# Performance work log

Hardware: AMD Instinct MI355X
Metric: run time of the kernel (lower is better)

Reference implementation:

```python
import jax, jax.numpy as jnp
import numpy as np

N = 50000
E = 800000
H = 128
L = 3
EPS_BN = 1e-5
EPS_NORM = 1e-12
NEG_SLOPE = 0.1


def setup_inputs() -> dict:
    key = jax.random.key(0)
    ks = jax.random.split(key, 10)
    s = 1.0 / np.sqrt(H)
    x = jax.random.normal(ks[0], (N, H), dtype=jnp.float32)
    edge_index = jax.random.randint(ks[1], (2, E), 0, N, dtype=jnp.int64)
    # per-layer SAGEConv params: lin_l (neighbors, with bias), lin_r (root, no bias)
    Wl = jax.random.uniform(ks[2], (L, H, H), jnp.float32, -s, s)
    bl = jax.random.uniform(ks[3], (L, H), jnp.float32, -s, s)
    Wr = jax.random.uniform(ks[4], (L, H, H), jnp.float32, -s, s)
    # BatchNorm affine params per layer
    gamma = jnp.ones((L, H), jnp.float32)
    beta = jnp.zeros((L, H), jnp.float32)
    # shared skip linear
    Ws = jax.random.uniform(ks[5], (H, H), jnp.float32, -s, s)
    bs = jax.random.uniform(ks[6], (H,), jnp.float32, -s, s)
    return {"x": x, "edge_index": edge_index, "Wl": Wl, "bl": bl, "Wr": Wr,
            "gamma": gamma, "beta": beta, "Ws": Ws, "bs": bs}


def _layer(x, src, dst, Wl, bl, Wr, g, b, Ws, bs):
    # skip residual
    res = x @ Ws.T + bs
    # SAGEConv mean aggregation: messages src -> dst
    agg = jax.ops.segment_sum(x[src], dst, num_segments=N)  # [N,H]
    deg = jax.ops.segment_sum(jnp.ones((E,), x.dtype), dst, num_segments=N)
    agg = agg / jnp.maximum(deg, 1.0)[:, None]
    out = agg @ Wl.T + bl + x @ Wr.T
    # normalize=True -> L2 normalize over features
    nrm = jnp.sqrt(jnp.sum(out * out, axis=-1, keepdims=True))
    out = out / jnp.maximum(nrm, EPS_NORM)
    # BatchNorm over nodes (batch statistics)
    mu = out.mean(axis=0)
    var = out.var(axis=0)
    out = (out - mu) * jax.lax.rsqrt(var + EPS_BN) * g + b
    # LeakyReLU(0.1); dropout is identity in eval
    out = jnp.where(out >= 0, out, NEG_SLOPE * out)
    return out + res


def reference(x, edge_index, Wl, bl, Wr, gamma, beta, Ws, bs):
    src, dst = edge_index[0], edge_index[1]
    for l in range(L):
        x = _layer(x, src, dst, Wl[l], bl[l], Wr[l], gamma[l], beta[l], Ws, bs)
    return x
```

## Files before the change

kernel.cpp:

```cpp
#include <hip/hip_runtime.h>
#include <hip/hip_bf16.h>
#include <stdint.h>

#define NN 50000
#define NE 800000
#define HD 128
#define NL 3
#define EPS_BN 1e-5f
#define EPS_NORM 1e-12f
#define NEG_SLOPE 0.1f

#define SCAN_CHUNK 256
#define SCAN_BLOCKS ((NN + SCAN_CHUNK - 1) / SCAN_CHUNK)
#define NTILES ((NN + 127) / 128)

#define BSH 9
#define NB ((NN + (1 << BSH) - 1) >> BSH)
#define MAXBE 9728

typedef __attribute__((ext_vector_type(8))) short bf16x8;
typedef __attribute__((ext_vector_type(4))) float f32x4;

static __device__ __forceinline__ unsigned pack_bf16(float a, float b) {
  unsigned ua = __builtin_bit_cast(unsigned, a);
  unsigned ub = __builtin_bit_cast(unsigned, b);
  ua = (ua + 0x7fffu + ((ua >> 16) & 1u)) >> 16;
  ub = (ub + 0x7fffu + ((ub >> 16) & 1u)) >> 16;
  return ua | (ub << 16);
}
static __device__ __forceinline__ ushort bf16of(float f) {
  unsigned u = __builtin_bit_cast(unsigned, f);
  u = (u + 0x7fffu + ((u >> 16) & 1u)) >> 16;
  return (ushort)u;
}
static __device__ __forceinline__ float bflo(unsigned u) { return __builtin_bit_cast(float, u << 16); }
static __device__ __forceinline__ float bfhi(unsigned u) { return __builtin_bit_cast(float, u & 0xffff0000u); }

__global__ __launch_bounds__(256) void hist_kernel(const int* __restrict__ dst, int* __restrict__ degi) {
  int i = blockIdx.x * 256 + threadIdx.x;
  if (i < NE) atomicAdd(&degi[dst[i]], 1);
}

__global__ __launch_bounds__(256) void blocksum_kernel(const int* __restrict__ degi,
                                                       int* __restrict__ blocksum) {
  __shared__ int sh[256];
  int t = threadIdx.x;
  int i = blockIdx.x * 256 + t;
  sh[t] = (i < NN) ? degi[i] : 0;
  __syncthreads();
  for (int off = 128; off >= 1; off >>= 1) {
    if (t < off) sh[t] += sh[t + off];
    __syncthreads();
  }
  if (t == 0) blocksum[blockIdx.x] = sh[0];
}

__global__ __launch_bounds__(256) void blockscan_kernel(int* __restrict__ blocksum,
                                                        int* __restrict__ blockoff,
                                                        int* __restrict__ rowptr) {
  __shared__ int sh[256];
  int t = threadIdx.x;
  int v = (t < SCAN_BLOCKS) ? blocksum[t] : 0;
  sh[t] = v;
  __syncthreads();
  for (int off = 1; off < 256; off <<= 1) {
    int u = (t >= off) ? sh[t - off] : 0;
    __syncthreads();
    sh[t] += u;
    __syncthreads();
  }
  if (t < SCAN_BLOCKS) blockoff[t] = sh[t] - v;
  if (t == 255) rowptr[NN] = sh[255];
}

__global__ __launch_bounds__(256) void chunkscan_kernel(const int* __restrict__ degi,
                                                        const int* __restrict__ blockoff,
                                                        int* __restrict__ rowptr,
                                                        int* __restrict__ bcursor,
                                                        float* __restrict__ invdeg) {
  __shared__ int sh[256];
  int t = threadIdx.x;
  int i = blockIdx.x * 256 + t;
  int d = (i < NN) ? degi[i] : 0;
  sh[t] = d;
  __syncthreads();
  for (int off = 1; off < 256; off <<= 1) {
    int u = (t >= off) ? sh[t - off] : 0;
    __syncthreads();
    sh[t] += u;
    __syncthreads();
  }
  if (i < NN) {
    int pre = blockoff[blockIdx.x] + sh[t] - d;
    rowptr[i] = pre;
    if ((i & ((1 << BSH) - 1)) == 0) bcursor[i >> BSH] = pre;
    invdeg[i] = 1.0f / fmaxf((float)d, 1.0f);
  }
}

__global__ __launch_bounds__(1024) void bucketB_kernel(const int* __restrict__ src,
                                                       const int* __restrict__ dst,
                                                       int* __restrict__ bcursor,
                                                       uint2* __restrict__ bpack) {
  __shared__ int hist[NB], lstart[NB], gbase[NB];
  __shared__ uint2 sdat[1024];
  const int tid = threadIdx.x;
  const int e = blockIdx.x * 1024 + tid;
  if (tid < NB) hist[tid] = 0;
  __syncthreads();
  int s = 0, d = 0, b = 0, myIdx = 0;
  bool valid = (e < NE);
  if (valid) {
    s = src[e];
    d = dst[e];
    b = d >> BSH;
    myIdx = atomicAdd(&hist[b], 1);
  }
  __syncthreads();
  if (tid == 0) {
    int run = 0;
    for (int i = 0; i < NB; ++i) { lstart[i] = run; run += hist[i]; }
  }
  __syncthreads();
  if (tid < NB && hist[tid] > 0) gbase[tid] = atomicAdd(&bcursor[tid], hist[tid]);
  __syncthreads();
  if (valid) sdat[lstart[b] + myIdx] = make_uint2((unsigned)s, (unsigned)d);
  __syncthreads();
  int tot = lstart[NB - 1] + hist[NB - 1];
  if (tid < tot) {
    uint2 p = sdat[tid];
    int bb = (int)(p.y >> BSH);
    bpack[gbase[bb] + (tid - lstart[bb])] = p;
  }
}

__global__ __launch_bounds__(1024) void bucketC_kernel(const int* __restrict__ rowptr,
                                                       const uint2* __restrict__ bpack,
                                                       int* __restrict__ esrc) {
  __shared__ int lcur[1 << BSH];
  __shared__ int lsrc[MAXBE];
  const int c = blockIdx.x, tid = threadIdx.x;
  const int nbase = c << BSH;
  const int nend = min(nbase + (1 << BSH), NN);
  const int ebase = rowptr[nbase];
  const int cnt = rowptr[nend] - ebase;
  if (tid < (1 << BSH)) {
    int n = nbase + tid;
    lcur[tid] = (n < nend) ? rowptr[n] - ebase : 0;
  }
  __syncthreads();
  for (int i = tid; i < cnt; i += 1024) {
    uint2 p = bpack[ebase + i];
    int pos = atomicAdd(&lcur[(int)p.y - nbase], 1);
    if (pos < MAXBE) lsrc[pos] = (int)p.x;
  }
  __syncthreads();
  for (int i = tid; i < cnt; i += 1024) esrc[ebase + i] = lsrc[i];
}

__global__ __launch_bounds__(256) void tobf16_kernel(const float* __restrict__ x, ushort* __restrict__ xb) {
  int i = blockIdx.x * 256 + threadIdx.x;
  if (i < NN * 64) {
    float2 f = *(const float2*)(x + (size_t)i * 2);
    *(unsigned*)(xb + (size_t)i * 2) = pack_bf16(f.x, f.y);
  }
}

__global__ __launch_bounds__(256) void packW_kernel(const float* __restrict__ Wl,
                                                    const float* __restrict__ Wr,
                                                    const float* __restrict__ Wsm,
                                                    unsigned* __restrict__ wpackL,
                                                    unsigned* __restrict__ wpackS) {
  int i = blockIdx.x * 256 + threadIdx.x;
  if (i < NL * 16384) {
    int l = i >> 14, rem = i & 16383;
    int c = rem >> 7, kp = rem & 127;
    int k2 = kp * 2;
    float f0, f1;
    if (k2 < HD) { const float* W = Wl + (size_t)l * HD * HD + c * HD + k2; f0 = W[0]; f1 = W[1]; }
    else         { const float* W = Wr + (size_t)l * HD * HD + c * HD + (k2 - HD); f0 = W[0]; f1 = W[1]; }
    unsigned ba = (unsigned)(c * 512 + kp * 4) ^ (unsigned)((c & 7) << 4);
    *(unsigned*)((char*)(wpackL + (size_t)l * 16384) + ba) = pack_bf16(f0, f1);
  } else if (i < NL * 16384 + 8192) {
    int j = i - NL * 16384;
    int c = j >> 6, kp = j & 63;
    int k2 = kp * 2;
    unsigned ba = (unsigned)(c * 256 + kp * 4) ^ (unsigned)((c & 7) << 4);
    *(unsigned*)((char*)wpackS + ba) = pack_bf16(Wsm[c * HD + k2], Wsm[c * HD + k2 + 1]);
  }
}

__global__ __launch_bounds__(512) void agg_csr_kernel(const ushort* __restrict__ xb,
                                                      const int* __restrict__ rowptr,
                                                      const int* __restrict__ esrc,
                                                      const float* __restrict__ invdeg,
                                                      ushort* __restrict__ aggb,
                                                      float* __restrict__ colsum,
                                                      float* __restrict__ colsumsq) {
  if (blockIdx.x == 0 && threadIdx.x < 2 * HD) {
    if (threadIdx.x < HD) colsum[threadIdx.x] = 0.f;
    else colsumsq[threadIdx.x - HD] = 0.f;
  }
  int wid = (blockIdx.x * 512 + threadIdx.x) >> 6;
  int lane = threadIdx.x & 63;
  int node = wid * 4 + (lane >> 4);
  int sub = lane & 15;
  if (node >= NN) return;
  int start = rowptr[node], end = rowptr[node + 1];
  float a0 = 0.f, a1 = 0.f, a2 = 0.f, a3 = 0.f, a4 = 0.f, a5 = 0.f, a6 = 0.f, a7 = 0.f;
  int e = start;
  for (; e + 4 <= end; e += 4) {
    int s0 = esrc[e], s1 = esrc[e + 1], s2 = esrc[e + 2], s3 = esrc[e + 3];
    uint4 u0 = *(const uint4*)((const char*)xb + (size_t)s0 * 256 + sub * 16);
    uint4 u1 = *(const uint4*)((const char*)xb + (size_t)s1 * 256 + sub * 16);
    uint4 u2 = *(const uint4*)((const char*)xb + (size_t)s2 * 256 + sub * 16);
    uint4 u3 = *(const uint4*)((const char*)xb + (size_t)s3 * 256 + sub * 16);
    a0 += (bflo(u0.x) + bflo(u1.x)) + (bflo(u2.x) + bflo(u3.x));
    a1 += (bfhi(u0.x) + bfhi(u1.x)) + (bfhi(u2.x) + bfhi(u3.x));
    a2 += (bflo(u0.y) + bflo(u1.y)) + (bflo(u2.y) + bflo(u3.y));
    a3 += (bfhi(u0.y) + bfhi(u1.y)) + (bfhi(u2.y) + bfhi(u3.y));
    a4 += (bflo(u0.z) + bflo(u1.z)) + (bflo(u2.z) + bflo(u3.z));
    a5 += (bfhi(u0.z) + bfhi(u1.z)) + (bfhi(u2.z) + bfhi(u3.z));
    a6 += (bflo(u0.w) + bflo(u1.w)) + (bflo(u2.w) + bflo(u3.w));
    a7 += (bfhi(u0.w) + bfhi(u1.w)) + (bfhi(u2.w) + bfhi(u3.w));
  }
  for (; e < end; ++e) {
    uint4 u = *(const uint4*)((const char*)xb + (size_t)esrc[e] * 256 + sub * 16);
    a0 += bflo(u.x); a1 += bfhi(u.x);
    a2 += bflo(u.y); a3 += bfhi(u.y);
    a4 += bflo(u.z); a5 += bfhi(u.z);
    a6 += bflo(u.w); a7 += bfhi(u.w);
  }
  float id = invdeg[node];
  uint4 o;
  o.x = pack_bf16(a0 * id, a1 * id);
  o.y = pack_bf16(a2 * id, a3 * id);
  o.z = pack_bf16(a4 * id, a5 * id);
  o.w = pack_bf16(a6 * id, a7 * id);
  *(uint4*)((char*)aggb + (size_t)node * 256 + sub * 16) = o;
}

__global__ __launch_bounds__(512, 4) void mfma_pre_kernel(
    const ushort* __restrict__ aggb, const ushort* __restrict__ xb,
    const unsigned* __restrict__ wpackL, const float* __restrict__ bl,
    uint4* __restrict__ prebn,
    float* __restrict__ colsum, float* __restrict__ colsumsq) {
  __shared__ unsigned Bsw[16384];
  __shared__ float lsum[HD], lsq[HD];
  const int tid = threadIdx.x;
  {
    const uint4* s = (const uint4*)wpackL;
    uint4* d = (uint4*)Bsw;
#pragma unroll
    for (int i = 0; i < 8; ++i) d[tid + i * 512] = s[tid + i * 512];
  }
  if (tid < HD) { lsum[tid] = 0.f; lsq[tid] = 0.f; }

  const int wave = tid >> 6, lane = tid & 63;
  const int lhi = lane >> 4, llo = lane & 15;
  int arow = blockIdx.x * 128 + wave * 16 + llo;
  if (arow >= NN) arow = NN - 1;
  const size_t rb = (size_t)arow * 256;

  uint4 areg[8];
#pragma unroll
  for (int ks = 0; ks < 4; ++ks) {
    areg[ks]     = *(const uint4*)((const char*)aggb + rb + ks * 64 + lhi * 16);
    areg[ks + 4] = *(const uint4*)((const char*)xb   + rb + ks * 64 + lhi * 16);
  }

  f32x4 acc[8];
#pragma unroll
  for (int ct = 0; ct < 8; ++ct) {
    float b = bl[ct * 16 + llo];
    acc[ct] = (f32x4){b, b, b, b};
  }
  __syncthreads();

#pragma unroll
  for (int ks = 0; ks < 8; ++ks) {
    bf16x8 a = __builtin_bit_cast(bf16x8, areg[ks]);
#pragma unroll
    for (int ct = 0; ct < 8; ++ct) {
      int bcol = ct * 16 + llo;
      unsigned bb = (unsigned)(bcol * 512 + ks * 64 + lhi * 16) ^ (unsigned)((bcol & 7) << 4);
      bf16x8 b = *(const bf16x8*)((const char*)Bsw + bb);
      acc[ct] = __builtin_amdgcn_mfma_f32_16x16x32_bf16(a, b, acc[ct], 0, 0, 0);
    }
  }

  float cs[8] = {0, 0, 0, 0, 0, 0, 0, 0}, cq[8] = {0, 0, 0, 0, 0, 0, 0, 0};
#pragma unroll
  for (int r = 0; r < 4; ++r) {
    int orow = blockIdx.x * 128 + wave * 16 + lhi * 4 + r;
    float p[8];
    float ss = 0.f;
#pragma unroll
    for (int ct = 0; ct < 8; ++ct) { p[ct] = acc[ct][r]; ss += p[ct] * p[ct]; }
#pragma unroll
    for (int m = 8; m >= 1; m >>= 1) ss += __shfl_xor(ss, m, 64);
    float inv = 1.0f / fmaxf(sqrtf(ss), EPS_NORM);
#pragma unroll
    for (int ct = 0; ct < 8; ++ct) p[ct] *= inv;
    uint4 o;
    o.x = pack_bf16(p[0], p[1]);
    o.y = pack_bf16(p[2], p[3]);
    o.z = pack_bf16(p[4], p[5]);
    o.w = pack_bf16(p[6], p[7]);
    prebn[((size_t)blockIdx.x * 32 + wave * 4 + r) * 64 + lane] = o;
    if (orow < NN) {
#pragma unroll
      for (int ct = 0; ct < 8; ++ct) { cs[ct] += p[ct]; cq[ct] += p[ct] * p[ct]; }
    }
  }
#pragma unroll
  for (int ct = 0; ct < 8; ++ct) {
    atomicAdd(&lsum[ct * 16 + llo], cs[ct]);
    atomicAdd(&lsq[ct * 16 + llo], cq[ct]);
  }
  __syncthreads();
  if (tid < HD) {
    atomicAdd(&colsum[tid], lsum[tid]);
    atomicAdd(&colsumsq[tid], lsq[tid]);
  }
}

__global__ __launch_bounds__(512, 4) void res_mfma_kernel(
    ushort* __restrict__ xb, const uint4* __restrict__ prebn,
    const unsigned* __restrict__ wpackS, const float* __restrict__ bs,
    const float* __restrict__ colsum, const float* __restrict__ colsumsq,
    const float* __restrict__ gamma, const float* __restrict__ beta,
    float* __restrict__ outf, int last) {
  __shared__ unsigned Bsw[8192];
  __shared__ float lscale[HD], lshift[HD];
  const int tid = threadIdx.x;
  {
    const uint4* s = (const uint4*)wpackS;
    uint4* d = (uint4*)Bsw;
#pragma unroll
    for (int i = 0; i < 4; ++i) d[tid + i * 512] = s[tid + i * 512];
  }
  if (tid < HD) {
    float mu = colsum[tid] * (1.0f / NN);
    float ex2 = colsumsq[tid] * (1.0f / NN);
    float var = ex2 - mu * mu;
    float sc = gamma[tid] * rsqrtf(var + EPS_BN);
    lscale[tid] = sc;
    lshift[tid] = beta[tid] - mu * sc;
  }

  const int wave = tid >> 6, lane = tid & 63;
  const int lhi = lane >> 4, llo = lane & 15;
  int arow = blockIdx.x * 128 + wave * 16 + llo;
  if (arow >= NN) arow = NN - 1;
  const size_t rb = (size_t)arow * 256;

  uint4 areg[4];
#pragma unroll
  for (int ks = 0; ks < 4; ++ks)
    areg[ks] = *(const uint4*)((const char*)xb + rb + ks * 64 + lhi * 16);
  uint4 pv4[4];
#pragma unroll
  for (int r = 0; r < 4; ++r)
    pv4[r] = prebn[((size_t)blockIdx.x * 32 + wave * 4 + r) * 64 + lane];

  f32x4 acc[8];
#pragma unroll
  for (int ct = 0; ct < 8; ++ct) {
    float b = bs[ct * 16 + llo];
    acc[ct] = (f32x4){b, b, b, b};
  }
  __syncthreads();

  float sc8[8], sh8[8];
#pragma unroll
  for (int ct = 0; ct < 8; ++ct) {
    int C = ct * 16 + llo;
    sc8[ct] = lscale[C];
    sh8[ct] = lshift[C];
  }

#pragma unroll
  for (int ks = 0; ks < 4; ++ks) {
    bf16x8 a = __builtin_bit_cast(bf16x8, areg[ks]);
#pragma unroll
    for (int ct = 0; ct < 8; ++ct) {
      int bcol = ct * 16 + llo;
      unsigned bb = (unsigned)(bcol * 256 + ks * 64 + lhi * 16) ^ (unsigned)((bcol & 7) << 4);
      bf16x8 b = *(const bf16x8*)((const char*)Bsw + bb);
      acc[ct] = __builtin_amdgcn_mfma_f32_16x16x32_bf16(a, b, acc[ct], 0, 0, 0);
    }
  }

#pragma unroll
  for (int r = 0; r < 4; ++r) {
    int orow = blockIdx.x * 128 + wave * 16 + lhi * 4 + r;
    if (orow < NN) {
      const unsigned* pw = (const unsigned*)&pv4[r];
#pragma unroll
      for (int ct = 0; ct < 8; ++ct) {
        unsigned w = pw[ct >> 1];
        float pv = (ct & 1) ? bfhi(w) : bflo(w);
        float v = pv * sc8[ct] + sh8[ct];
        v = v >= 0.f ? v : NEG_SLOPE * v;
        float o = v + acc[ct][r];
        if (last) outf[(size_t)orow * HD + ct * 16 + llo] = o;
        else      xb[(size_t)orow * HD + ct * 16 + llo] = bf16of(o);
      }
    }
  }
}

extern "C" void kernel_launch(void* const* d_in, const int* in_sizes, int n_in,
                              void* d_out, int out_size, void* d_ws, size_t ws_size,
                              hipStream_t stream) {
  const float* x0    = (const float*)d_in[0];
  const int*   ei    = (const int*)d_in[1];
  const float* Wl    = (const float*)d_in[2];
  const float* bl    = (const float*)d_in[3];
  const float* Wr    = (const float*)d_in[4];
  const float* gamma = (const float*)d_in[5];
  const float* beta  = (const float*)d_in[6];
  const float* Wsm   = (const float*)d_in[7];
  const float* bs    = (const float*)d_in[8];
  float* out = (float*)d_out;

  char* w = (char*)d_ws;
  ushort* aggb = (ushort*)w;        w += (size_t)NN * HD * 2;
  ushort* xb   = (ushort*)w;        w += (size_t)NN * HD * 2;
  uint4* prebn = (uint4*)w;         w += (size_t)NTILES * 32 * 64 * 16;
  unsigned* wpackL = (unsigned*)w;  w += (size_t)NL * 16384 * 4;
  unsigned* wpackS = (unsigned*)w;  w += 8192 * 4;
  float* invdeg = (float*)w;        w += (size_t)NN * 4;
  float* colsum = (float*)w;        w += HD * 4;
  float* colsumsq = (float*)w;      w += HD * 4;
  int* degi = (int*)w;              w += (size_t)NN * 4;
  int* rowptr = (int*)w;            w += (size_t)(NN + 1) * 4;
  int* bcursor = (int*)w;           w += (size_t)(NB + 8) * 4;
  int* blocksum = (int*)w;          w += SCAN_BLOCKS * 4;
  int* blockoff = (int*)w;          w += SCAN_BLOCKS * 4;
  uint2* bpack = (uint2*)w;         w += (size_t)NE * 8;
  int* esrc = (int*)w;              w += (size_t)NE * 4;

  const int* srcp = ei;
  const int* dstp = ei + NE;

  hipMemsetAsync(degi, 0, NN * sizeof(int), stream);
  hist_kernel<<<(NE + 255) / 256, 256, 0, stream>>>(dstp, degi);
  blocksum_kernel<<<SCAN_BLOCKS, 256, 0, stream>>>(degi, blocksum);
  blockscan_kernel<<<1, 256, 0, stream>>>(blocksum, blockoff, rowptr);
  chunkscan_kernel<<<SCAN_BLOCKS, 256, 0, stream>>>(degi, blockoff, rowptr, bcursor, invdeg);
  bucketB_kernel<<<(NE + 1023) / 1024, 1024, 0, stream>>>(srcp, dstp, bcursor, bpack);
  bucketC_kernel<<<NB, 1024, 0, stream>>>(rowptr, bpack, esrc);
  tobf16_kernel<<<(NN * 64 + 255) / 256, 256, 0, stream>>>(x0, xb);
  packW_kernel<<<(NL * 16384 + 8192 + 255) / 256, 256, 0, stream>>>(Wl, Wr, Wsm, wpackL, wpackS);

  const int aggBlocks = (((NN + 3) / 4) * 64 + 511) / 512;
  for (int l = 0; l < NL; ++l) {
    agg_csr_kernel<<<aggBlocks, 512, 0, stream>>>(xb, rowptr, esrc, invdeg, aggb,
                                                  colsum, colsumsq);
    mfma_pre_kernel<<<NTILES, 512, 0, stream>>>(aggb, xb, wpackL + (size_t)l * 16384,
                                                bl + (size_t)l * HD, prebn, colsum, colsumsq);
    res_mfma_kernel<<<NTILES, 512, 0, stream>>>(xb, prebn, wpackS, bs,
                                                colsum, colsumsq,
                                                gamma + (size_t)l * HD, beta + (size_t)l * HD,
                                                out, l == NL - 1 ? 1 : 0);
  }
}
```

Baseline: 306.9 us.

## Fuse CSR neighbor aggregation into the MFMA pre-BN kernel via shared memory

The separate aggregation kernel is removed. Each 128-row tile block now gathers its neighbor means directly into the first half of its shared buffer, with an XOR swizzle, and then loads its A operands from there. This drops the global write and re-read of the bf16 aggregate buffer and one launch per layer. The second half of the weights is staged first, and the first half is loaded after the aggregate tile has been consumed, which adds an extra barrier. Column-sum zeroing moves to one upfront memset of per-layer stats buffers. Fewer gather waves run concurrently, since the block count is now limited to one block per tile, which could hurt latency hiding for the irregular gathers.

```diff
diff --git a/kernel.cpp b/kernel.cpp
--- a/kernel.cpp
+++ b/kernel.cpp
@@ -190,83 +190,92 @@
   }
 }
 
-__global__ __launch_bounds__(512) void agg_csr_kernel(const ushort* __restrict__ xb,
-                                                      const int* __restrict__ rowptr,
-                                                      const int* __restrict__ esrc,
-                                                      const float* __restrict__ invdeg,
-                                                      ushort* __restrict__ aggb,
-                                                      float* __restrict__ colsum,
-                                                      float* __restrict__ colsumsq) {
-  if (blockIdx.x == 0 && threadIdx.x < 2 * HD) {
-    if (threadIdx.x < HD) colsum[threadIdx.x] = 0.f;
-    else colsumsq[threadIdx.x - HD] = 0.f;
-  }
-  int wid = (blockIdx.x * 512 + threadIdx.x) >> 6;
-  int lane = threadIdx.x & 63;
-  int node = wid * 4 + (lane >> 4);
-  int sub = lane & 15;
-  if (node >= NN) return;
-  int start = rowptr[node], end = rowptr[node + 1];
-  float a0 = 0.f, a1 = 0.f, a2 = 0.f, a3 = 0.f, a4 = 0.f, a5 = 0.f, a6 = 0.f, a7 = 0.f;
-  int e = start;
-  for (; e + 4 <= end; e += 4) {
-    int s0 = esrc[e], s1 = esrc[e + 1], s2 = esrc[e + 2], s3 = esrc[e + 3];
-    uint4 u0 = *(const uint4*)((const char*)xb + (size_t)s0 * 256 + sub * 16);
-    uint4 u1 = *(const uint4*)((const char*)xb + (size_t)s1 * 256 + sub * 16);
-    uint4 u2 = *(const uint4*)((const char*)xb + (size_t)s2 * 256 + sub * 16);
-    uint4 u3 = *(const uint4*)((const char*)xb + (size_t)s3 * 256 + sub * 16);
-    a0 += (bflo(u0.x) + bflo(u1.x)) + (bflo(u2.x) + bflo(u3.x));
-    a1 += (bfhi(u0.x) + bfhi(u1.x)) + (bfhi(u2.x) + bfhi(u3.x));
-    a2 += (bflo(u0.y) + bflo(u1.y)) + (bflo(u2.y) + bflo(u3.y));
-    a3 += (bfhi(u0.y) + bfhi(u1.y)) + (bfhi(u2.y) + bfhi(u3.y));
-    a4 += (bflo(u0.z) + bflo(u1.z)) + (bflo(u2.z) + bflo(u3.z));
-    a5 += (bfhi(u0.z) + bfhi(u1.z)) + (bfhi(u2.z) + bfhi(u3.z));
-    a6 += (bflo(u0.w) + bflo(u1.w)) + (bflo(u2.w) + bflo(u3.w));
-    a7 += (bfhi(u0.w) + bfhi(u1.w)) + (bfhi(u2.w) + bfhi(u3.w));
-  }
-  for (; e < end; ++e) {
-    uint4 u = *(const uint4*)((const char*)xb + (size_t)esrc[e] * 256 + sub * 16);
-    a0 += bflo(u.x); a1 += bfhi(u.x);
-    a2 += bflo(u.y); a3 += bfhi(u.y);
-    a4 += bflo(u.z); a5 += bfhi(u.z);
-    a6 += bflo(u.w); a7 += bfhi(u.w);
-  }
-  float id = invdeg[node];
-  uint4 o;
-  o.x = pack_bf16(a0 * id, a1 * id);
-  o.y = pack_bf16(a2 * id, a3 * id);
-  o.z = pack_bf16(a4 * id, a5 * id);
-  o.w = pack_bf16(a6 * id, a7 * id);
-  *(uint4*)((char*)aggb + (size_t)node * 256 + sub * 16) = o;
-}
-
-__global__ __launch_bounds__(512, 4) void mfma_pre_kernel(
-    const ushort* __restrict__ aggb, const ushort* __restrict__ xb,
+__global__ __launch_bounds__(512, 4) void fused_pre_kernel(
+    const ushort* __restrict__ xb, const int* __restrict__ rowptr,
+    const int* __restrict__ esrc, const float* __restrict__ invdeg,
     const unsigned* __restrict__ wpackL, const float* __restrict__ bl,
     uint4* __restrict__ prebn,
     float* __restrict__ colsum, float* __restrict__ colsumsq) {
   __shared__ unsigned Bsw[16384];
   __shared__ float lsum[HD], lsq[HD];
   const int tid = threadIdx.x;
+  const int r0 = blockIdx.x * 128;
+
   {
     const uint4* s = (const uint4*)wpackL;
     uint4* d = (uint4*)Bsw;
 #pragma unroll
-    for (int i = 0; i < 8; ++i) d[tid + i * 512] = s[tid + i * 512];
+    for (int i = 0; i < 4; ++i) d[2048 + tid + i * 512] = s[2048 + tid + i * 512];
   }
   if (tid < HD) { lsum[tid] = 0.f; lsq[tid] = 0.f; }
 
   const int wave = tid >> 6, lane = tid & 63;
+
+  {
+    const int sub = lane & 15;
+#pragma unroll
+    for (int pass = 0; pass < 4; ++pass) {
+      int nl = pass * 32 + wave * 4 + (lane >> 4);
+      int node = r0 + nl;
+      uint4 o = make_uint4(0u, 0u, 0u, 0u);
+      if (node < NN) {
+        int start = rowptr[node], end = rowptr[node + 1];
+        float a0 = 0.f, a1 = 0.f, a2 = 0.f, a3 = 0.f, a4 = 0.f, a5 = 0.f, a6 = 0.f, a7 = 0.f;
+        int e = start;
+        for (; e + 4 <= end; e += 4) {
+          int s0 = esrc[e], s1 = esrc[e + 1], s2 = esrc[e + 2], s3 = esrc[e + 3];
+          uint4 u0 = *(const uint4*)((const char*)xb + (size_t)s0 * 256 + sub * 16);
+          uint4 u1 = *(const uint4*)((const char*)xb + (size_t)s1 * 256 + sub * 16);
+          uint4 u2 = *(const uint4*)((const char*)xb + (size_t)s2 * 256 + sub * 16);
+          uint4 u3 = *(const uint4*)((const char*)xb + (size_t)s3 * 256 + sub * 16);
+          a0 += (bflo(u0.x) + bflo(u1.x)) + (bflo(u2.x) + bflo(u3.x));
+          a1 += (bfhi(u0.x) + bfhi(u1.x)) + (bfhi(u2.x) + bfhi(u3.x));
+          a2 += (bflo(u0.y) + bflo(u1.y)) + (bflo(u2.y) + bflo(u3.y));
+          a3 += (bfhi(u0.y) + bfhi(u1.y)) + (bfhi(u2.y) + bfhi(u3.y));
+          a4 += (bflo(u0.z) + bflo(u1.z)) + (bflo(u2.z) + bflo(u3.z));
+          a5 += (bfhi(u0.z) + bfhi(u1.z)) + (bfhi(u2.z) + bfhi(u3.z));
+          a6 += (bflo(u0.w) + bflo(u1.w)) + (bflo(u2.w) + bflo(u3.w));
+          a7 += (bfhi(u0.w) + bfhi(u1.w)) + (bfhi(u2.w) + bfhi(u3.w));
+        }
+        for (; e < end; ++e) {
+          uint4 u = *(const uint4*)((const char*)xb + (size_t)esrc[e] * 256 + sub * 16);
+          a0 += bflo(u.x); a1 += bfhi(u.x);
+          a2 += bflo(u.y); a3 += bfhi(u.y);
+          a4 += bflo(u.z); a5 += bfhi(u.z);
+          a6 += bflo(u.w); a7 += bfhi(u.w);
+        }
+        float id = invdeg[node];
+        o.x = pack_bf16(a0 * id, a1 * id);
+        o.y = pack_bf16(a2 * id, a3 * id);
+        o.z = pack_bf16(a4 * id, a5 * id);
+        o.w = pack_bf16(a6 * id, a7 * id);
+      }
+      unsigned ba = (unsigned)(nl * 256 + ((sub ^ (nl & 7)) * 16));
+      *(uint4*)((char*)Bsw + ba) = o;
+    }
+  }
+  __syncthreads();
+
   const int lhi = lane >> 4, llo = lane & 15;
-  int arow = blockIdx.x * 128 + wave * 16 + llo;
+  const int rl = wave * 16 + llo;
+  int arow = r0 + rl;
   if (arow >= NN) arow = NN - 1;
   const size_t rb = (size_t)arow * 256;
 
   uint4 areg[8];
 #pragma unroll
   for (int ks = 0; ks < 4; ++ks) {
-    areg[ks]     = *(const uint4*)((const char*)aggb + rb + ks * 64 + lhi * 16);
-    areg[ks + 4] = *(const uint4*)((const char*)xb   + rb + ks * 64 + lhi * 16);
+    unsigned ba = (unsigned)(rl * 256 + (((ks * 4 + lhi) ^ (rl & 7)) * 16));
+    areg[ks] = *(const uint4*)((const char*)Bsw + ba);
+    areg[ks + 4] = *(const uint4*)((const char*)xb + rb + ks * 64 + lhi * 16);
+  }
+  __syncthreads();
+
+  {
+    const uint4* s = (const uint4*)wpackL;
+    uint4* d = (uint4*)Bsw;
+#pragma unroll
+    for (int i = 0; i < 4; ++i) d[tid + i * 512] = s[tid + i * 512];
   }
 
   f32x4 acc[8];
@@ -292,7 +301,7 @@
   float cs[8] = {0, 0, 0, 0, 0, 0, 0, 0}, cq[8] = {0, 0, 0, 0, 0, 0, 0, 0};
 #pragma unroll
   for (int r = 0; r < 4; ++r) {
-    int orow = blockIdx.x * 128 + wave * 16 + lhi * 4 + r;
+    int orow = r0 + wave * 16 + lhi * 4 + r;
     float p[8];
     float ss = 0.f;
 #pragma unroll
@@ -426,14 +435,12 @@
   float* out = (float*)d_out;
 
   char* w = (char*)d_ws;
-  ushort* aggb = (ushort*)w;        w += (size_t)NN * HD * 2;
   ushort* xb   = (ushort*)w;        w += (size_t)NN * HD * 2;
   uint4* prebn = (uint4*)w;         w += (size_t)NTILES * 32 * 64 * 16;
   unsigned* wpackL = (unsigned*)w;  w += (size_t)NL * 16384 * 4;
   unsigned* wpackS = (unsigned*)w;  w += 8192 * 4;
   float* invdeg = (float*)w;        w += (size_t)NN * 4;
-  float* colsum = (float*)w;        w += HD * 4;
-  float* colsumsq = (float*)w;      w += HD * 4;
+  float* colsums = (float*)w;       w += (size_t)NL * 2 * HD * 4;
   int* degi = (int*)w;              w += (size_t)NN * 4;
   int* rowptr = (int*)w;            w += (size_t)(NN + 1) * 4;
   int* bcursor = (int*)w;           w += (size_t)(NB + 8) * 4;
@@ -446,6 +453,7 @@
   const int* dstp = ei + NE;
 
   hipMemsetAsync(degi, 0, NN * sizeof(int), stream);
+  hipMemsetAsync(colsums, 0, (size_t)NL * 2 * HD * sizeof(float), stream);
   hist_kernel<<<(NE + 255) / 256, 256, 0, stream>>>(dstp, degi);
   blocksum_kernel<<<SCAN_BLOCKS, 256, 0, stream>>>(degi, blocksum);
   blockscan_kernel<<<1, 256, 0, stream>>>(blocksum, blockoff, rowptr);
@@ -455,12 +463,13 @@
   tobf16_kernel<<<(NN * 64 + 255) / 256, 256, 0, stream>>>(x0, xb);
   packW_kernel<<<(NL * 16384 + 8192 + 255) / 256, 256, 0, stream>>>(Wl, Wr, Wsm, wpackL, wpackS);
 
-  const int aggBlocks = (((NN + 3) / 4) * 64 + 511) / 512;
   for (int l = 0; l < NL; ++l) {
-    agg_csr_kernel<<<aggBlocks, 512, 0, stream>>>(xb, rowptr, esrc, invdeg, aggb,
-                                                  colsum, colsumsq);
-    mfma_pre_kernel<<<NTILES, 512, 0, stream>>>(aggb, xb, wpackL + (size_t)l * 16384,
-                                                bl + (size_t)l * HD, prebn, colsum, colsumsq);
+    float* colsum = colsums + (size_t)l * 2 * HD;
+    float* colsumsq = colsum + HD;
+    fused_pre_kernel<<<NTILES, 512, 0, stream>>>(xb, rowptr, esrc, invdeg,
+                                                 wpackL + (size_t)l * 16384,
+                                                 bl + (size_t)l * HD, prebn,
+                                                 colsum, colsumsq);
     res_mfma_kernel<<<NTILES, 512, 0, stream>>>(xb, prebn, wpackS, bs,
                                                 colsum, colsumsq,
                                                 gamma + (size_t)l * HD, beta + (size_t)l * HD,
```

Measured after the change: 310.3 us. Within noise of the previous version (+1.1%).
